# Kernel tuning notes

Hardware: AMD Instinct MI355X
Metric: run time of the kernel (lower is better)

Reference implementation:

```python
import jax, jax.numpy as jnp
import numpy as np

B, U, C, M = 4096, 1024, 5000, 20

def setup_inputs() -> dict:
    key = jax.random.key(0)
    ks = jax.random.split(key, 9)
    inputs = jax.random.randint(ks[0], (B, 1), 0, C).astype(jnp.int32)
    states = 0.1 * jax.random.normal(ks[1], (B, U + 2), dtype=jnp.float32)
    bias_z = jnp.zeros((U,), jnp.float32)
    recurrent_kernel = 0.02 * jax.random.normal(ks[2], (U, 4 * U), dtype=jnp.float32)
    kernel_c = 0.02 * jax.random.normal(ks[3], (C, 4 * U), dtype=jnp.float32)
    bias = jnp.zeros((3 * U,), jnp.float32)
    kernel_d = 0.1 * jax.random.normal(ks[4], (2, 4 * U), dtype=jnp.float32)
    Wgmm_part1 = 0.05 * jax.random.normal(ks[5], (U, 3 * M), dtype=jnp.float32)
    bgmm_part1 = jnp.zeros((3 * M,), jnp.float32)
    return {"inputs": inputs, "states": states, "bias_z": bias_z,
            "recurrent_kernel": recurrent_kernel, "kernel_c": kernel_c,
            "bias": bias, "kernel_d": kernel_d,
            "Wgmm_part1": Wgmm_part1, "bgmm_part1": bgmm_part1}

def exp_safe(x):
    return jnp.clip(jnp.exp(x), 1e-10, 1e10)

def reference(inputs, states, bias_z, recurrent_kernel, kernel_c, bias,
              kernel_d, Wgmm_part1, bgmm_part1):
    u = bias_z.shape[0]
    h_tm1 = states[:, :-2]          # [B, U]
    _d = states[:, -2:]             # [B, 2]
    ch = inputs[:, 0].astype(jnp.int32)
    # one_hot(ch) @ kernel_c is just a row gather
    pre = kernel_c[ch] + _d @ kernel_d              # [B, 4U]
    # z and r gates share the left operand -> fuse into one matmul
    zr = (h_tm1 @ recurrent_kernel[:, :2 * u] + pre[:, :2 * u]
          + jnp.concatenate([bias_z, bias[:u]]))
    z = jax.nn.sigmoid(zr[:, :u])
    r = jax.nn.sigmoid(zr[:, u:])
    hh = jnp.tanh((r * h_tm1) @ recurrent_kernel[:, 2 * u:3 * u]
                  + pre[:, 2 * u:3 * u] + bias[u:2 * u])
    h = z * h_tm1 + (1.0 - z) * hh
    o = jnp.tanh(h @ recurrent_kernel[:, 3 * u:]
                 + pre[:, 3 * u:] + bias[2 * u:])
    gmm = o @ Wgmm_part1 + bgmm_part1               # [B, 3M]
    _pi, mux, muy = jnp.split(gmm, 3, axis=-1)
    e = exp_safe(_pi)
    pi = e / jnp.sum(e, axis=-1, keepdims=True)
    x_pred = jnp.sum(pi * mux, axis=-1, keepdims=True)
    y_pred = jnp.sum(pi * muy, axis=-1, keepdims=True)
    out = jnp.concatenate([o, pi, mux, muy, x_pred, y_pred], axis=-1)
    new_state = jnp.concatenate([h, x_pred, y_pred], axis=-1)
    return out, new_state
```

## Files before the change

### kernel.cpp

```cpp
#include <hip/hip_runtime.h>

typedef __attribute__((ext_vector_type(8))) short     bf16x8;
typedef __attribute__((ext_vector_type(4))) float     f32x4;
typedef __attribute__((ext_vector_type(2))) float     f32x2;
typedef __attribute__((ext_vector_type(4))) unsigned short u16x4;

#define OUT_STRIDE 1086
#define NS_STRIDE 1026
#define NS_BASE (4096*1086)

__device__ __forceinline__ unsigned short f2bf(float x) {
  unsigned int u = __float_as_uint(x);
  unsigned int r = (u + 0x7FFFu + ((u >> 16) & 1u)) >> 16;
  return (unsigned short)r;
}
__device__ __forceinline__ float bf2f(unsigned short u) {
  union { unsigned int i; float f; } v; v.i = ((unsigned int)u) << 16; return v.f;
}
__device__ __forceinline__ float sigmoidf(float x) { return 1.f / (1.f + expf(-x)); }

__device__ __forceinline__ void gld_lds16(const void* g, void* l) {
  __builtin_amdgcn_global_load_lds((const __attribute__((address_space(1))) void*)g,
                                   (__attribute__((address_space(3))) void*)l, 16, 0, 0);
}

__global__ __launch_bounds__(256)
void transposeR(const float* __restrict__ R, unsigned short* __restrict__ Bt) {
  __shared__ float t[64][65];
  const int tx = threadIdx.x & 63, ty = threadIdx.x >> 6;
  const int j0 = blockIdx.x * 64, k0 = blockIdx.y * 64;
#pragma unroll
  for (int i = 0; i < 64; i += 4)
    t[ty + i][tx] = R[(size_t)(k0 + ty + i) * 4096 + j0 + tx];
  __syncthreads();
#pragma unroll
  for (int i = 0; i < 64; i += 4) {
    const int j = ty + i;
    Bt[(size_t)(j0 + j) * 1024 + k0 + tx] = f2bf(t[tx][j]);
  }
}

__global__ __launch_bounds__(256)
void convertH(const float* __restrict__ states, unsigned short* __restrict__ hb) {
  const int idx = blockIdx.x * 256 + threadIdx.x;
  const int b = idx >> 8, u = (idx & 255) * 4;
  const float* sp = states + (size_t)b * 1026 + u;
  f32x2 v0 = *(const f32x2*)sp, v1 = *(const f32x2*)(sp + 2);
  u16x4 w;
  w[0] = f2bf(v0[0]); w[1] = f2bf(v0[1]); w[2] = f2bf(v1[0]); w[3] = f2bf(v1[1]);
  *(u16x4*)&hb[(size_t)b * 1024 + u] = w;
}

template<int EPI, int NTN>
__global__ __launch_bounds__(256, 2)
void gemm_bt(const unsigned short* __restrict__ A,
             const unsigned short* __restrict__ Bt, int colbase,
             const int* __restrict__ chv,
             const float* __restrict__ states,
             const float* __restrict__ kcm,
             const float* __restrict__ kd,
             const float* __restrict__ bias_z,
             const float* __restrict__ bias,
             float* __restrict__ zbuf,
             unsigned short* __restrict__ rh,
             float* __restrict__ outp,
             unsigned short* __restrict__ hb2) {
  __shared__ __align__(16) char ldsb[65536];
  __shared__ int   chs[128];
  __shared__ float d0s[128], d1s[128];

  const int tid = threadIdx.x, lane = tid & 63, wave = tid >> 6;
  const int wr = wave >> 1, wc = wave & 1;
  const int arow = lane & 15, q = lane >> 4;
  const int bid = blockIdx.x;

  int mt, nt;
  if (NTN == 16) {
    const int swz = (bid & 7) * 64 + (bid >> 3);
    const int chunk = swz >> 6, l = swz & 63;
    mt = (chunk & 3) * 8 + (l >> 3);
    nt = (chunk >> 2) * 8 + (l & 7);
  } else {
    const int xcd = bid & 7, j = bid >> 3;
    mt = xcd * 4 + (j >> 3);
    nt = j & 7;
  }
  const int m0 = mt * 128, n0 = nt * 128;

  if (tid < 128) {
    const int r = m0 + tid;
    chs[tid] = chv[r];
    d0s[tid] = states[(size_t)r * 1026 + 1024];
    d1s[tid] = states[(size_t)r * 1026 + 1025];
  }

  const unsigned short* Ag = A  + (size_t)m0 * 1024;
  const unsigned short* Bg = Bt + (size_t)(colbase + n0) * 1024;

  f32x4 acc[4][4] = {};

#define ST1(c, G, Loff, kk) {                                                  \
    const int row_ = (c) >> 2;                                                 \
    const int ss_  = ((c) & 3) ^ (row_ & 3);                                   \
    gld_lds16(G + (size_t)row_ * 1024 + (kk) + ss_ * 8, ldsb + (Loff) + (c) * 16); }
#define STAGE(b, kk) {                                                         \
    ST1(tid,       Ag, (b) * 8192,         kk)                                 \
    ST1(tid + 256, Ag, (b) * 8192,         kk)                                 \
    ST1(tid,       Bg, 32768 + (b) * 8192, kk)                                 \
    ST1(tid + 256, Bg, 32768 + (b) * 8192, kk) }

  const int sq = (q ^ (arow & 3)) << 4;

  auto compute = [&](int cb) {
    bf16x8 af[4], bfr[4];
    const char* Ab = ldsb + cb * 8192;
    const char* Bb = ldsb + 32768 + cb * 8192;
#pragma unroll
    for (int mi = 0; mi < 4; ++mi) {
      const int R = wr * 64 + mi * 16 + arow;
      af[mi] = *(const bf16x8*)(Ab + R * 64 + sq);
    }
#pragma unroll
    for (int ni = 0; ni < 4; ++ni) {
      const int R = wc * 64 + ni * 16 + arow;
      bfr[ni] = *(const bf16x8*)(Bb + R * 64 + sq);
    }
    __builtin_amdgcn_s_setprio(1);
#pragma unroll
    for (int mi = 0; mi < 4; ++mi)
#pragma unroll
      for (int ni = 0; ni < 4; ++ni)
        acc[mi][ni] = __builtin_amdgcn_mfma_f32_16x16x32_bf16(af[mi], bfr[ni], acc[mi][ni], 0, 0, 0);
    __builtin_amdgcn_s_setprio(0);
  };

  STAGE(0, 0)
  STAGE(1, 32)
  for (int t = 0; t < 30; ++t) {
    STAGE((t + 2) & 3, (t + 2) * 32)
    asm volatile("s_waitcnt vmcnt(8)" ::: "memory");
    __builtin_amdgcn_s_barrier();
    asm volatile("" ::: "memory");
    compute(t & 3);
  }
  asm volatile("s_waitcnt vmcnt(4)" ::: "memory");
  __builtin_amdgcn_s_barrier();
  asm volatile("" ::: "memory");
  compute(2);
  asm volatile("s_waitcnt vmcnt(0)" ::: "memory");
  __builtin_amdgcn_s_barrier();
  asm volatile("" ::: "memory");
  compute(3);
#undef STAGE
#undef ST1

#pragma unroll
  for (int mi = 0; mi < 4; ++mi) {
#pragma unroll
    for (int i = 0; i < 4; ++i) {
      const int lrow = wr * 64 + mi * 16 + q * 4 + i;
      const int grow = m0 + lrow;
      const int ch = chs[lrow];
      const float d0 = d0s[lrow], d1 = d1s[lrow];
      const float* kcr = kcm + (size_t)ch * 4096;
#pragma unroll
      for (int ni = 0; ni < 4; ++ni) {
        const int gc = n0 + wc * 64 + ni * 16 + arow;
        const float a = acc[mi][ni][i];
        if (EPI == 1) {
          const int fullc = gc;
          const float pre = kcr[fullc] + d0 * kd[fullc] + d1 * kd[4096 + fullc];
          if (n0 < 1024) {
            const float z = sigmoidf(a + pre + bias_z[gc]);
            zbuf[(size_t)grow * 1024 + gc] = z;
          } else {
            const int uc = gc - 1024;
            const float r = sigmoidf(a + pre + bias[uc]);
            rh[(size_t)grow * 1024 + uc] = f2bf(r * states[(size_t)grow * 1026 + uc]);
          }
        } else if (EPI == 2) {
          const int fullc = 2048 + gc;
          const float v = a + kcr[fullc] + d0 * kd[fullc] + d1 * kd[4096 + fullc] + bias[1024 + gc];
          const float hh = tanhf(v);
          const float z = zbuf[(size_t)grow * 1024 + gc];
          const float htm = states[(size_t)grow * 1026 + gc];
          const float h = z * htm + (1.f - z) * hh;
          outp[(size_t)grow * NS_STRIDE + gc] = h;
          hb2[(size_t)grow * 1024 + gc] = f2bf(h);
        } else {
          const int fullc = 3072 + gc;
          const float v = a + kcr[fullc] + d0 * kd[fullc] + d1 * kd[4096 + fullc] + bias[2048 + gc];
          outp[(size_t)grow * OUT_STRIDE + gc] = tanhf(v);
        }
      }
    }
  }
}

__global__ __launch_bounds__(512)
void gmm_kernel(const float* __restrict__ obuf,
                const float* __restrict__ Wg,
                const float* __restrict__ bg,
                float* __restrict__ outp,
                float* __restrict__ ns) {
  __shared__ float Wl[128 * 60 + 16];
  __shared__ float ol[8 * 1024];
  const int tid = threadIdx.x;
  const int lane = tid & 63;
  const int wave = tid >> 6;
  const int row0 = blockIdx.x * 8;

  for (int i = tid; i < 4096; i += 512) {
    const int rr = i >> 9, c2 = (i & 511) * 2;
    *(f32x2*)&ol[rr * 1024 + c2] = *(const f32x2*)&obuf[(size_t)(row0 + rr) * OUT_STRIDE + c2];
  }

  float g = 0.f;
  for (int kc0 = 0; kc0 < 1024; kc0 += 128) {
    __syncthreads();
    for (int i = tid; i < 1920; i += 512)
      *(f32x4*)&Wl[i * 4] = *(const f32x4*)&Wg[kc0 * 60 + i * 4];
    __syncthreads();
    const float* orow = &ol[wave * 1024 + kc0];
#pragma unroll 8
    for (int k = 0; k < 128; ++k)
      g = fmaf(orow[k], Wl[k * 60 + lane], g);
  }
  if (lane < 60) g += bg[lane];

  float e = 0.f;
  if (lane < 20) e = fminf(fmaxf(expf(g), 1e-10f), 1e10f);
  float s = e;
#pragma unroll
  for (int m = 1; m < 32; m <<= 1) s += __shfl_xor(s, m, 64);
  const float pi = (lane < 20) ? e / s : 0.f;
  const int src1 = (lane < 20) ? lane + 20 : lane;
  const int src2 = (lane < 20) ? lane + 40 : lane;
  const float mux = __shfl(g, src1, 64);
  const float muy = __shfl(g, src2, 64);
  float px = pi * mux, py = pi * muy;
#pragma unroll
  for (int m = 1; m < 32; m <<= 1) { px += __shfl_xor(px, m, 64); py += __shfl_xor(py, m, 64); }

  const int row = row0 + wave;
  float* orow = outp + (size_t)row * OUT_STRIDE;
  if (lane < 20) orow[1024 + lane] = pi;
  else if (lane < 60) orow[1024 + lane] = g;
  if (lane == 0) {
    orow[1084] = px;
    orow[1085] = py;
    ns[(size_t)row * NS_STRIDE + 1024] = px;
    ns[(size_t)row * NS_STRIDE + 1025] = py;
  }
}

extern "C" void kernel_launch(void* const* d_in, const int* in_sizes, int n_in,
                              void* d_out, int out_size, void* d_ws, size_t ws_size,
                              hipStream_t stream) {
  const int*   chv    = (const int*)d_in[0];
  const float* states = (const float*)d_in[1];
  const float* bias_z = (const float*)d_in[2];
  const float* R      = (const float*)d_in[3];
  const float* kc     = (const float*)d_in[4];
  const float* bias   = (const float*)d_in[5];
  const float* kd     = (const float*)d_in[6];
  const float* Wg     = (const float*)d_in[7];
  const float* bg     = (const float*)d_in[8];
  float* out = (float*)d_out;

  char* ws = (char*)d_ws;
  unsigned short* RbT  = (unsigned short*)ws;
  unsigned short* hb   = (unsigned short*)(ws + 8388608);
  unsigned short* rh   = (unsigned short*)(ws + 16777216);
  unsigned short* hb2  = (unsigned short*)(ws + 25165824);
  float*          zbuf = (float*)(ws + 33554432);

  transposeR<<<dim3(64, 16), 256, 0, stream>>>(R, RbT);
  convertH<<<4096, 256, 0, stream>>>(states, hb);

  gemm_bt<1, 16><<<512, 256, 0, stream>>>(hb, RbT, 0,
      chv, states, kc, kd, bias_z, bias, zbuf, rh, nullptr, nullptr);

  gemm_bt<2, 8><<<256, 256, 0, stream>>>(rh, RbT, 2048,
      chv, states, kc, kd, bias_z, bias, zbuf, nullptr, out + NS_BASE, hb2);

  gemm_bt<3, 8><<<256, 256, 0, stream>>>(hb2, RbT, 3072,
      chv, states, kc, kd, bias_z, bias, nullptr, nullptr, out, nullptr);

  gmm_kernel<<<512, 512, 0, stream>>>(out, Wg, bg, out, out + NS_BASE);
}
```

Baseline: 357.0 us.

## Replace LDS-staged block GEMM with single-wave direct-global-load GEMM tiles

Swaps the 256-thread, 128x128-tile GEMM that staged A and B through LDS with a 4-deep global_load_lds pipeline for a one-wave, 64x64-tile kernel. The new kernel loads MFMA fragments straight from global memory into registers, double-buffered, and launches four times as many blocks with a new XCD-aware tile mapping. This removes LDS traffic and block barriers and raises block count. In exchange it loses the cross-wave data reuse a shared LDS tile gives, so it relies more on L2 bandwidth and issues uncoalesced-pattern fragment loads.

```diff
diff --git a/kernel.cpp b/kernel.cpp
--- a/kernel.cpp
+++ b/kernel.cpp
@@ -18,11 +18,6 @@
   union { unsigned int i; float f; } v; v.i = ((unsigned int)u) << 16; return v.f;
 }
 __device__ __forceinline__ float sigmoidf(float x) { return 1.f / (1.f + expf(-x)); }
-
-__device__ __forceinline__ void gld_lds16(const void* g, void* l) {
-  __builtin_amdgcn_global_load_lds((const __attribute__((address_space(1))) void*)g,
-                                   (__attribute__((address_space(3))) void*)l, 16, 0, 0);
-}
 
 __global__ __launch_bounds__(256)
 void transposeR(const float* __restrict__ R, unsigned short* __restrict__ Bt) {
@@ -51,125 +46,91 @@
   *(u16x4*)&hb[(size_t)b * 1024 + u] = w;
 }
 
-template<int EPI, int NTN>
-__global__ __launch_bounds__(256, 2)
-void gemm_bt(const unsigned short* __restrict__ A,
-             const unsigned short* __restrict__ Bt, int colbase,
-             const int* __restrict__ chv,
-             const float* __restrict__ states,
-             const float* __restrict__ kcm,
-             const float* __restrict__ kd,
-             const float* __restrict__ bias_z,
-             const float* __restrict__ bias,
-             float* __restrict__ zbuf,
-             unsigned short* __restrict__ rh,
-             float* __restrict__ outp,
-             unsigned short* __restrict__ hb2) {
-  __shared__ __align__(16) char ldsb[65536];
-  __shared__ int   chs[128];
-  __shared__ float d0s[128], d1s[128];
-
-  const int tid = threadIdx.x, lane = tid & 63, wave = tid >> 6;
-  const int wr = wave >> 1, wc = wave & 1;
+template<int EPI, int NBLK>
+__global__ __launch_bounds__(64, 2)
+void gemm_w(const unsigned short* __restrict__ A,
+            const unsigned short* __restrict__ Bt, int colbase,
+            const int* __restrict__ chv,
+            const float* __restrict__ states,
+            const float* __restrict__ kcm,
+            const float* __restrict__ kd,
+            const float* __restrict__ bias_z,
+            const float* __restrict__ bias,
+            float* __restrict__ zbuf,
+            unsigned short* __restrict__ rh,
+            float* __restrict__ outp,
+            unsigned short* __restrict__ hb2) {
+  __shared__ int   chs[64];
+  __shared__ float d0s[64], d1s[64];
+
+  const int lane = threadIdx.x;
   const int arow = lane & 15, q = lane >> 4;
-  const int bid = blockIdx.x;
 
   int mt, nt;
-  if (NTN == 16) {
-    const int swz = (bid & 7) * 64 + (bid >> 3);
-    const int chunk = swz >> 6, l = swz & 63;
-    mt = (chunk & 3) * 8 + (l >> 3);
-    nt = (chunk >> 2) * 8 + (l & 7);
-  } else {
-    const int xcd = bid & 7, j = bid >> 3;
-    mt = xcd * 4 + (j >> 3);
-    nt = j & 7;
-  }
-  const int m0 = mt * 128, n0 = nt * 128;
-
-  if (tid < 128) {
-    const int r = m0 + tid;
-    chs[tid] = chv[r];
-    d0s[tid] = states[(size_t)r * 1026 + 1024];
-    d1s[tid] = states[(size_t)r * 1026 + 1025];
-  }
-
-  const unsigned short* Ag = A  + (size_t)m0 * 1024;
-  const unsigned short* Bg = Bt + (size_t)(colbase + n0) * 1024;
+  {
+    const int xcd = blockIdx.x & 7, l = blockIdx.x >> 3;
+    const int cm = xcd >> 1, cn = xcd & 1;
+    if (NBLK == 2048) {
+      mt = cm * 16 + (l & 15);
+      nt = cn * 16 + (l >> 4);
+    } else {
+      mt = cm * 16 + (l & 15);
+      nt = cn * 8 + (l >> 4);
+    }
+  }
+  const int m0 = mt * 64, n0 = nt * 64;
+
+  chs[lane] = chv[m0 + lane];
+  d0s[lane] = states[(size_t)(m0 + lane) * 1026 + 1024];
+  d1s[lane] = states[(size_t)(m0 + lane) * 1026 + 1025];
+  __syncthreads();
+
+  const unsigned short* Al = A  + (size_t)(m0 + arow) * 1024 + q * 8;
+  const unsigned short* Bl = Bt + (size_t)(colbase + n0 + arow) * 1024 + q * 8;
 
   f32x4 acc[4][4] = {};
-
-#define ST1(c, G, Loff, kk) {                                                  \
-    const int row_ = (c) >> 2;                                                 \
-    const int ss_  = ((c) & 3) ^ (row_ & 3);                                   \
-    gld_lds16(G + (size_t)row_ * 1024 + (kk) + ss_ * 8, ldsb + (Loff) + (c) * 16); }
-#define STAGE(b, kk) {                                                         \
-    ST1(tid,       Ag, (b) * 8192,         kk)                                 \
-    ST1(tid + 256, Ag, (b) * 8192,         kk)                                 \
-    ST1(tid,       Bg, 32768 + (b) * 8192, kk)                                 \
-    ST1(tid + 256, Bg, 32768 + (b) * 8192, kk) }
-
-  const int sq = (q ^ (arow & 3)) << 4;
-
-  auto compute = [&](int cb) {
-    bf16x8 af[4], bfr[4];
-    const char* Ab = ldsb + cb * 8192;
-    const char* Bb = ldsb + 32768 + cb * 8192;
-#pragma unroll
-    for (int mi = 0; mi < 4; ++mi) {
-      const int R = wr * 64 + mi * 16 + arow;
-      af[mi] = *(const bf16x8*)(Ab + R * 64 + sq);
-    }
-#pragma unroll
-    for (int ni = 0; ni < 4; ++ni) {
-      const int R = wc * 64 + ni * 16 + arow;
-      bfr[ni] = *(const bf16x8*)(Bb + R * 64 + sq);
-    }
-    __builtin_amdgcn_s_setprio(1);
-#pragma unroll
-    for (int mi = 0; mi < 4; ++mi)
-#pragma unroll
-      for (int ni = 0; ni < 4; ++ni)
-        acc[mi][ni] = __builtin_amdgcn_mfma_f32_16x16x32_bf16(af[mi], bfr[ni], acc[mi][ni], 0, 0, 0);
-    __builtin_amdgcn_s_setprio(0);
-  };
-
-  STAGE(0, 0)
-  STAGE(1, 32)
-  for (int t = 0; t < 30; ++t) {
-    STAGE((t + 2) & 3, (t + 2) * 32)
-    asm volatile("s_waitcnt vmcnt(8)" ::: "memory");
-    __builtin_amdgcn_s_barrier();
-    asm volatile("" ::: "memory");
-    compute(t & 3);
-  }
-  asm volatile("s_waitcnt vmcnt(4)" ::: "memory");
-  __builtin_amdgcn_s_barrier();
-  asm volatile("" ::: "memory");
-  compute(2);
-  asm volatile("s_waitcnt vmcnt(0)" ::: "memory");
-  __builtin_amdgcn_s_barrier();
-  asm volatile("" ::: "memory");
-  compute(3);
-#undef STAGE
-#undef ST1
+  bf16x8 a0[4], b0[4], a1[4], b1[4];
+
+#define LOADF(AF, BF, kk) {                                                    \
+    _Pragma("unroll")                                                          \
+    for (int mi = 0; mi < 4; ++mi)                                             \
+      AF[mi] = *(const bf16x8*)(Al + (size_t)mi * 16384 + (kk));               \
+    _Pragma("unroll")                                                          \
+    for (int ni = 0; ni < 4; ++ni)                                             \
+      BF[ni] = *(const bf16x8*)(Bl + (size_t)ni * 16384 + (kk)); }
+#define MM(AF, BF) {                                                           \
+    _Pragma("unroll")                                                          \
+    for (int mi = 0; mi < 4; ++mi)                                             \
+      _Pragma("unroll")                                                        \
+      for (int ni = 0; ni < 4; ++ni)                                           \
+        acc[mi][ni] = __builtin_amdgcn_mfma_f32_16x16x32_bf16(AF[mi], BF[ni], acc[mi][ni], 0, 0, 0); }
+
+  LOADF(a0, b0, 0)
+#pragma unroll
+  for (int t = 0; t < 32; t += 2) {
+    if (t + 1 < 32) LOADF(a1, b1, (t + 1) * 32)
+    MM(a0, b0)
+    if (t + 2 < 32) LOADF(a0, b0, (t + 2) * 32)
+    if (t + 1 < 32) MM(a1, b1)
+  }
+#undef LOADF
+#undef MM
 
 #pragma unroll
   for (int mi = 0; mi < 4; ++mi) {
 #pragma unroll
     for (int i = 0; i < 4; ++i) {
-      const int lrow = wr * 64 + mi * 16 + q * 4 + i;
+      const int lrow = mi * 16 + q * 4 + i;
       const int grow = m0 + lrow;
       const int ch = chs[lrow];
       const float d0 = d0s[lrow], d1 = d1s[lrow];
       const float* kcr = kcm + (size_t)ch * 4096;
 #pragma unroll
       for (int ni = 0; ni < 4; ++ni) {
-        const int gc = n0 + wc * 64 + ni * 16 + arow;
+        const int gc = n0 + ni * 16 + arow;
         const float a = acc[mi][ni][i];
         if (EPI == 1) {
-          const int fullc = gc;
-          const float pre = kcr[fullc] + d0 * kd[fullc] + d1 * kd[4096 + fullc];
+          const float pre = kcr[gc] + d0 * kd[gc] + d1 * kd[4096 + gc];
           if (n0 < 1024) {
             const float z = sigmoidf(a + pre + bias_z[gc]);
             zbuf[(size_t)grow * 1024 + gc] = z;
@@ -278,13 +239,13 @@
   transposeR<<<dim3(64, 16), 256, 0, stream>>>(R, RbT);
   convertH<<<4096, 256, 0, stream>>>(states, hb);
 
-  gemm_bt<1, 16><<<512, 256, 0, stream>>>(hb, RbT, 0,
+  gemm_w<1, 2048><<<2048, 64, 0, stream>>>(hb, RbT, 0,
       chv, states, kc, kd, bias_z, bias, zbuf, rh, nullptr, nullptr);
 
-  gemm_bt<2, 8><<<256, 256, 0, stream>>>(rh, RbT, 2048,
+  gemm_w<2, 1024><<<1024, 64, 0, stream>>>(rh, RbT, 2048,
       chv, states, kc, kd, bias_z, bias, zbuf, nullptr, out + NS_BASE, hb2);
 
-  gemm_bt<3, 8><<<256, 256, 0, stream>>>(hb2, RbT, 3072,
+  gemm_w<3, 1024><<<1024, 64, 0, stream>>>(hb2, RbT, 3072,
       chv, states, kc, kd, bias_z, bias, nullptr, nullptr, out, nullptr);
 
   gmm_kernel<<<512, 512, 0, stream>>>(out, Wg, bg, out, out + NS_BASE);
```

Result: slower. 443.0 us (+24.1%).
